# Kernel tuning notes

Hardware: AMD Instinct MI355X
Metric: run time of the kernel (lower is better)

Reference implementation:

```python
import jax, jax.numpy as jnp
import numpy as np

N_NODES = 8192
K = 64


def setup_inputs() -> dict:
    key = jax.random.key(0)
    k1, k2 = jax.random.split(key)
    A = jax.random.normal(k1, (N_NODES, N_NODES), dtype=jnp.float32)
    idx = jax.random.randint(k2, (N_NODES,), 0, N_NODES, dtype=jnp.int64)
    return {"A": A, "idx": idx}


def reference(A, idx):
    # adj = relu(A)
    adj = jax.nn.relu(A)
    # per-row top-k indices (dim=1), then scatter a 0/1 mask and multiply
    _, ind = jax.lax.top_k(adj, K)  # ind: [N, K]
    rows = jnp.arange(adj.shape[0], dtype=ind.dtype)[:, None]  # [N, 1]
    mask = jnp.zeros_like(adj).at[rows, ind].set(1.0)
    return adj * mask
```

## Files before the change

### kernel.cpp

```cpp
#include <hip/hip_runtime.h>
#include <stdint.h>


constexpr int N      = 8192;
constexpr int K      = 64;
constexpr int BLOCK  = 256;
constexpr int VPT    = N / BLOCK;
constexpr int V4     = VPT / 4;
constexpr int CAP    = 1536;
constexpr int EQ_CAP = 256;

__device__ __forceinline__ uint32_t wave_reduce_add(uint32_t x) {
    #pragma unroll
    for (int d = 32; d >= 1; d >>= 1) x += __shfl_down(x, d, 64);
    return x;
}

__device__ __forceinline__ void scan_pick(const uint32_t* hist256,
                                          uint32_t* s_prefix, uint32_t* s_k,
                                          int shift, int lane) {
    uint32_t k  = *s_k;
    uint32_t h0 = hist256[4 * lane + 0];
    uint32_t h1 = hist256[4 * lane + 1];
    uint32_t h2 = hist256[4 * lane + 2];
    uint32_t h3 = hist256[4 * lane + 3];
    uint32_t suf = h0 + h1 + h2 + h3;
    #pragma unroll
    for (int d = 1; d < 64; d <<= 1) {
        uint32_t o = __shfl_down(suf, d, 64);
        if (lane + d < 64) suf += o;
    }
    unsigned long long m = __ballot(suf >= k);
    int cl = 63 - __builtin_clzll(m);
    if (lane == cl) {
        uint32_t S0 = suf, S1 = S0 - h0, S2 = S1 - h1, S3 = S2 - h2;
        int b; uint32_t Sb, hb;
        if      (S3 >= k) { b = 3; Sb = S3; hb = h3; }
        else if (S2 >= k) { b = 2; Sb = S2; hb = h2; }
        else if (S1 >= k) { b = 1; Sb = S1; hb = h1; }
        else              { b = 0; Sb = S0; hb = h0; }
        *s_prefix |= (uint32_t)(4 * lane + b) << shift;
        *s_k = k - (Sb - hb);
    }
}

__global__ __launch_bounds__(BLOCK) void topk_row_kernel(
    const float* __restrict__ A, float* __restrict__ out)
{
    __shared__ uint32_t hist[4][256];
    __shared__ uint32_t list[CAP];
    __shared__ uint32_t s_eq[EQ_CAP];
    __shared__ uint32_t s_rb[4][5];
    __shared__ uint32_t s_rmax[4];
    __shared__ uint32_t s_prefix, s_k, s_cnt, s_listcnt, s_C, s_ecut, s_mode, s_max;

    const int tid  = threadIdx.x;
    const int wave = tid >> 6;
    const int lane = tid & 63;
    const int row  = blockIdx.x;

    const float4* rowp = reinterpret_cast<const float4*>(A + (size_t)row * N);
    float4*       outp = reinterpret_cast<float4*>(out + (size_t)row * N);

    uint32_t v[VPT];
    #pragma unroll
    for (int j = 0; j < V4; ++j) {
        float4 f = rowp[tid + j * BLOCK];
        v[4*j+0] = (f.x > 0.f) ? __float_as_uint(f.x) : 0u;
        v[4*j+1] = (f.y > 0.f) ? __float_as_uint(f.y) : 0u;
        v[4*j+2] = (f.z > 0.f) ? __float_as_uint(f.z) : 0u;
        v[4*j+3] = (f.w > 0.f) ? __float_as_uint(f.w) : 0u;
    }
    if (tid == 0) { s_listcnt = 0; s_cnt = 0; }

    uint32_t mx = 0;
    #pragma unroll
    for (int j = 0; j < VPT; ++j) mx = (v[j] > mx) ? v[j] : mx;
    #pragma unroll
    for (int d = 32; d >= 1; d >>= 1) {
        uint32_t o = __shfl_down(mx, d, 64);
        mx = (o > mx) ? o : mx;
    }
    if (lane == 0) s_rmax[wave] = mx;
    __syncthreads();
    if (tid == 0) {
        uint32_t m = s_rmax[0];
        m = (s_rmax[1] > m) ? s_rmax[1] : m;
        m = (s_rmax[2] > m) ? s_rmax[2] : m;
        m = (s_rmax[3] > m) ? s_rmax[3] : m;
        s_max = m;
    }
    __syncthreads();
    const uint32_t expM = s_max >> 23;

    uint32_t b0 = 0, b1 = 0, b2 = 0, b3 = 0, cpos = 0;
    #pragma unroll
    for (int j = 0; j < VPT; ++j) {
        uint32_t x = v[j];
        if (x != 0u) {
            uint32_t d = expM - (x >> 23);
            cpos += 1u;
            b0 += (d == 0u); b1 += (d == 1u); b2 += (d == 2u); b3 += (d == 3u);
        }
    }
    b0 = wave_reduce_add(b0); b1 = wave_reduce_add(b1);
    b2 = wave_reduce_add(b2); b3 = wave_reduce_add(b3);
    cpos = wave_reduce_add(cpos);
    if (lane == 0) {
        s_rb[wave][0] = b0; s_rb[wave][1] = b1; s_rb[wave][2] = b2;
        s_rb[wave][3] = b3; s_rb[wave][4] = cpos;
    }
    __syncthreads();
    if (tid == 0) {
        uint32_t B[5];
        #pragma unroll
        for (int c = 0; c < 5; ++c)
            B[c] = s_rb[0][c] + s_rb[1][c] + s_rb[2][c] + s_rb[3][c];
        if (B[4] < (uint32_t)K) {
            s_mode = 1;
        } else {
            s_mode = 0;
            uint32_t cum = 0; int jf = -1;
            #pragma unroll
            for (int j = 0; j < 4; ++j) {
                cum += B[j];
                if (jf < 0 && cum >= (uint32_t)K) jf = j;
            }
            if (jf >= 0) {
                uint32_t c2 = 0;
                for (int j = 0; j <= jf; ++j) c2 += B[j];
                s_C = c2; s_ecut = expM - (uint32_t)jf;
            } else {
                s_C = 0;
            }
        }
    }
    __syncthreads();

    if (s_mode == 1) {
        #pragma unroll
        for (int j = 0; j < V4; ++j) {
            float4 o;
            o.x = __uint_as_float(v[4*j+0]); o.y = __uint_as_float(v[4*j+1]);
            o.z = __uint_as_float(v[4*j+2]); o.w = __uint_as_float(v[4*j+3]);
            outp[tid + j * BLOCK] = o;
        }
        return;
    }

    if (s_C == 0) {
        uint32_t ecut = (expM > 7u) ? (expM - 7u) : 0u;
        for (;;) {
            __syncthreads();
            uint32_t lc = 0;
            #pragma unroll
            for (int j = 0; j < VPT; ++j)
                lc += (v[j] != 0u && (v[j] >> 23) >= ecut) ? 1u : 0u;
            lc = wave_reduce_add(lc);
            if (lane == 0) s_rb[wave][0] = lc;
            __syncthreads();
            if (tid == 0) {
                s_C = s_rb[0][0] + s_rb[1][0] + s_rb[2][0] + s_rb[3][0];
                s_ecut = ecut;
            }
            __syncthreads();
            if (s_C >= (uint32_t)K || ecut == 0u) break;
            ecut = (ecut > 4u) ? (ecut - 4u) : 0u;
        }
    }
    __syncthreads();
    const uint32_t C    = s_C;
    const uint32_t ecut = s_ecut;

    #pragma unroll
    for (int c = 0; c < 4; ++c) hist[c][tid] = 0;
    if (tid == 0) { s_prefix = 0; s_k = K; }
    __syncthreads();

    if (C <= (uint32_t)CAP) {
        uint32_t lc = 0;
        #pragma unroll
        for (int j = 0; j < VPT; ++j)
            lc += (v[j] != 0u && (v[j] >> 23) >= ecut) ? 1u : 0u;
        uint32_t incl = lc;
        #pragma unroll
        for (int d = 1; d < 64; d <<= 1) {
            uint32_t t = __shfl_up(incl, d, 64);
            if (lane >= d) incl += t;
        }
        uint32_t baseV = 0;
        if (lane == 63) baseV = atomicAdd(&s_listcnt, incl);
        uint32_t base = __shfl(baseV, 63, 64);
        uint32_t pos  = base + (incl - lc);
        #pragma unroll
        for (int j = 0; j < VPT; ++j) {
            uint32_t x = v[j];
            if (x != 0u && (x >> 23) >= ecut) list[pos++] = x;
        }
        __syncthreads();

        for (uint32_t i = tid; i < C; i += BLOCK)
            atomicAdd(&hist[wave][list[i] >> 24], 1u);
        __syncthreads();
        hist[0][tid] = hist[0][tid] + hist[1][tid] + hist[2][tid] + hist[3][tid];
        __syncthreads();
        if (wave == 0) scan_pick(hist[0], &s_prefix, &s_k, 24, lane);
        __syncthreads();

        for (int shift = 16; shift >= 0; shift -= 8) {
            const uint32_t prefix = s_prefix;
            #pragma unroll
            for (int c = 0; c < 4; ++c) hist[c][tid] = 0;
            __syncthreads();
            const uint32_t himask = 0xFFFFFFFFu << (shift + 8);
            for (uint32_t i = tid; i < C; i += BLOCK) {
                uint32_t x = list[i];
                if ((x & himask) == prefix)
                    atomicAdd(&hist[wave][(x >> shift) & 255u], 1u);
            }
            __syncthreads();
            hist[0][tid] = hist[0][tid] + hist[1][tid] + hist[2][tid] + hist[3][tid];
            __syncthreads();
            if (wave == 0) scan_pick(hist[0], &s_prefix, &s_k, shift, lane);
            __syncthreads();
        }
    } else {
        #pragma unroll
        for (int j = 0; j < VPT; ++j) {
            uint32_t x = v[j];
            if (x) atomicAdd(&hist[wave][x >> 24], 1u);
        }
        __syncthreads();
        hist[0][tid] = hist[0][tid] + hist[1][tid] + hist[2][tid] + hist[3][tid];
        __syncthreads();
        if (wave == 0) scan_pick(hist[0], &s_prefix, &s_k, 24, lane);
        __syncthreads();

        for (int shift = 16; shift >= 0; shift -= 8) {
            const uint32_t prefix = s_prefix;
            #pragma unroll
            for (int c = 0; c < 4; ++c) hist[c][tid] = 0;
            __syncthreads();
            const uint32_t himask = 0xFFFFFFFFu << (shift + 8);
            #pragma unroll
            for (int j = 0; j < VPT; ++j) {
                uint32_t x = v[j];
                if ((x & himask) == prefix)
                    atomicAdd(&hist[wave][(x >> shift) & 255u], 1u);
            }
            __syncthreads();
            hist[0][tid] = hist[0][tid] + hist[1][tid] + hist[2][tid] + hist[3][tid];
            __syncthreads();
            if (wave == 0) scan_pick(hist[0], &s_prefix, &s_k, shift, lane);
            __syncthreads();
        }
    }

    const uint32_t T    = s_prefix;
    const uint32_t need = s_k;
    const float    Tf   = __uint_as_float(T);

    #pragma unroll
    for (int j = 0; j < V4; ++j) {
        const int base = (tid + j * BLOCK) * 4;
        float4 o;
        float* oc = &o.x;
        #pragma unroll
        for (int c = 0; c < 4; ++c) {
            uint32_t x = v[4*j+c];
            float val = 0.f;
            if (x > T) {
                val = __uint_as_float(x);
            } else if (x == T) {
                uint32_t p = atomicAdd(&s_cnt, 1u);
                if (p < (uint32_t)EQ_CAP) s_eq[p] = (uint32_t)(base + c);
            }
            oc[c] = val;
        }
        outp[tid + j * BLOCK] = o;
    }
    __syncthreads();

    if (tid == 0) {
        uint32_t cnt = s_cnt < (uint32_t)EQ_CAP ? s_cnt : (uint32_t)EQ_CAP;
        for (uint32_t n = 0; n < need; ++n) {
            uint32_t best = 0xFFFFFFFFu, bi = 0;
            for (uint32_t i = 0; i < cnt; ++i)
                if (s_eq[i] < best) { best = s_eq[i]; bi = i; }
            if (best != 0xFFFFFFFFu) {
                s_eq[bi] = 0xFFFFFFFFu;
                out[(size_t)row * N + best] = Tf;
            }
        }
    }
}

extern "C" void kernel_launch(void* const* d_in, const int* in_sizes, int n_in,
                              void* d_out, int out_size, void* d_ws, size_t ws_size,
                              hipStream_t stream) {
    const float* A = (const float*)d_in[0];
    float* out = (float*)d_out;
    topk_row_kernel<<<N, BLOCK, 0, stream>>>(A, out);
}
```

Baseline: 442.9 us.

## Replace candidate radix passes with rank-counting threshold selection and 512-thread blocks

The small-candidate path now finds the k-th largest threshold by having each thread count how many list entries exceed its own candidate, replacing three radix-histogram passes and their barriers. Blocks grow to 512 threads with occupancy hints, row loads become nontemporal, and the per-wave reductions are folded into shared atomics with packed 16-bit counters. The cost is O(C) comparisons per thread over shared memory, and the candidate cap is lowered to 1024 so the rank path handles at most two candidates per thread.

```diff
diff --git a/kernel.cpp b/kernel.cpp
--- a/kernel.cpp
+++ b/kernel.cpp
@@ -4,11 +4,13 @@
 
 constexpr int N      = 8192;
 constexpr int K      = 64;
-constexpr int BLOCK  = 256;
+constexpr int BLOCK  = 512;
 constexpr int VPT    = N / BLOCK;
 constexpr int V4     = VPT / 4;
-constexpr int CAP    = 1536;
+constexpr int CAP    = 1024;
 constexpr int EQ_CAP = 256;
+
+typedef float  fx4 __attribute__((ext_vector_type(4)));
 
 __device__ __forceinline__ uint32_t wave_reduce_add(uint32_t x) {
     #pragma unroll
@@ -44,34 +46,39 @@
     }
 }
 
-__global__ __launch_bounds__(BLOCK) void topk_row_kernel(
+__global__ __launch_bounds__(BLOCK, 6) void topk_row_kernel(
     const float* __restrict__ A, float* __restrict__ out)
 {
+    __shared__ uint32_t list[CAP];
     __shared__ uint32_t hist[4][256];
-    __shared__ uint32_t list[CAP];
     __shared__ uint32_t s_eq[EQ_CAP];
-    __shared__ uint32_t s_rb[4][5];
-    __shared__ uint32_t s_rmax[4];
-    __shared__ uint32_t s_prefix, s_k, s_cnt, s_listcnt, s_C, s_ecut, s_mode, s_max;
+    __shared__ uint32_t s_wred[8];
+    __shared__ uint32_t s_B[5];
+    __shared__ uint32_t s_max, s_listcnt, s_cnt, s_mode, s_C, s_ecut, s_T, s_need;
 
     const int tid  = threadIdx.x;
     const int wave = tid >> 6;
     const int lane = tid & 63;
     const int row  = blockIdx.x;
 
-    const float4* rowp = reinterpret_cast<const float4*>(A + (size_t)row * N);
-    float4*       outp = reinterpret_cast<float4*>(out + (size_t)row * N);
+    const fx4* rowp = reinterpret_cast<const fx4*>(A + (size_t)row * N);
+    float4*    outp = reinterpret_cast<float4*>(out + (size_t)row * N);
+
+    if (tid == 0) {
+        s_max = 0; s_listcnt = 0; s_cnt = 0; s_mode = 0;
+        s_T = 0xFFFFFFFFu; s_need = 0;
+    }
+    if (tid < 5) s_B[tid] = 0;
 
     uint32_t v[VPT];
     #pragma unroll
     for (int j = 0; j < V4; ++j) {
-        float4 f = rowp[tid + j * BLOCK];
+        fx4 f = __builtin_nontemporal_load(&rowp[tid + j * BLOCK]);
         v[4*j+0] = (f.x > 0.f) ? __float_as_uint(f.x) : 0u;
         v[4*j+1] = (f.y > 0.f) ? __float_as_uint(f.y) : 0u;
         v[4*j+2] = (f.z > 0.f) ? __float_as_uint(f.z) : 0u;
         v[4*j+3] = (f.w > 0.f) ? __float_as_uint(f.w) : 0u;
     }
-    if (tid == 0) { s_listcnt = 0; s_cnt = 0; }
 
     uint32_t mx = 0;
     #pragma unroll
@@ -81,58 +88,48 @@
         uint32_t o = __shfl_down(mx, d, 64);
         mx = (o > mx) ? o : mx;
     }
-    if (lane == 0) s_rmax[wave] = mx;
+    __syncthreads();
+    if (lane == 0) atomicMax(&s_max, mx);
+    __syncthreads();
+    const uint32_t expM = s_max >> 23;
+
+    {
+        uint32_t p01 = 0, p23 = 0, cp = 0;
+        #pragma unroll
+        for (int j = 0; j < VPT; ++j) {
+            uint32_t x = v[j];
+            if (x != 0u) {
+                uint32_t d = expM - (x >> 23);
+                cp  += 1u;
+                p01 += (d == 0u ? 1u : 0u) + (d == 1u ? 0x10000u : 0u);
+                p23 += (d == 2u ? 1u : 0u) + (d == 3u ? 0x10000u : 0u);
+            }
+        }
+        p01 = wave_reduce_add(p01);
+        p23 = wave_reduce_add(p23);
+        cp  = wave_reduce_add(cp);
+        if (lane == 0) {
+            atomicAdd(&s_B[0], p01 & 0xFFFFu);
+            atomicAdd(&s_B[1], p01 >> 16);
+            atomicAdd(&s_B[2], p23 & 0xFFFFu);
+            atomicAdd(&s_B[3], p23 >> 16);
+            atomicAdd(&s_B[4], cp);
+        }
+    }
     __syncthreads();
     if (tid == 0) {
-        uint32_t m = s_rmax[0];
-        m = (s_rmax[1] > m) ? s_rmax[1] : m;
-        m = (s_rmax[2] > m) ? s_rmax[2] : m;
-        m = (s_rmax[3] > m) ? s_rmax[3] : m;
-        s_max = m;
-    }
-    __syncthreads();
-    const uint32_t expM = s_max >> 23;
-
-    uint32_t b0 = 0, b1 = 0, b2 = 0, b3 = 0, cpos = 0;
-    #pragma unroll
-    for (int j = 0; j < VPT; ++j) {
-        uint32_t x = v[j];
-        if (x != 0u) {
-            uint32_t d = expM - (x >> 23);
-            cpos += 1u;
-            b0 += (d == 0u); b1 += (d == 1u); b2 += (d == 2u); b3 += (d == 3u);
-        }
-    }
-    b0 = wave_reduce_add(b0); b1 = wave_reduce_add(b1);
-    b2 = wave_reduce_add(b2); b3 = wave_reduce_add(b3);
-    cpos = wave_reduce_add(cpos);
-    if (lane == 0) {
-        s_rb[wave][0] = b0; s_rb[wave][1] = b1; s_rb[wave][2] = b2;
-        s_rb[wave][3] = b3; s_rb[wave][4] = cpos;
-    }
-    __syncthreads();
-    if (tid == 0) {
-        uint32_t B[5];
-        #pragma unroll
-        for (int c = 0; c < 5; ++c)
-            B[c] = s_rb[0][c] + s_rb[1][c] + s_rb[2][c] + s_rb[3][c];
-        if (B[4] < (uint32_t)K) {
+        if (s_B[4] < (uint32_t)K) {
             s_mode = 1;
         } else {
-            s_mode = 0;
             uint32_t cum = 0; int jf = -1;
             #pragma unroll
             for (int j = 0; j < 4; ++j) {
-                cum += B[j];
-                if (jf < 0 && cum >= (uint32_t)K) jf = j;
-            }
-            if (jf >= 0) {
-                uint32_t c2 = 0;
-                for (int j = 0; j <= jf; ++j) c2 += B[j];
-                s_C = c2; s_ecut = expM - (uint32_t)jf;
-            } else {
-                s_C = 0;
-            }
+                cum += s_B[j];
+                if (jf < 0 && cum >= (uint32_t)K) {
+                    jf = j; s_C = cum; s_ecut = expM - (uint32_t)j;
+                }
+            }
+            if (jf < 0) s_mode = 2;
         }
     }
     __syncthreads();
@@ -148,34 +145,30 @@
         return;
     }
 
-    if (s_C == 0) {
-        uint32_t ecut = (expM > 7u) ? (expM - 7u) : 0u;
+    if (s_mode == 2) {
+        uint32_t ec = (expM > 7u) ? (expM - 7u) : 0u;
         for (;;) {
             __syncthreads();
             uint32_t lc = 0;
             #pragma unroll
             for (int j = 0; j < VPT; ++j)
-                lc += (v[j] != 0u && (v[j] >> 23) >= ecut) ? 1u : 0u;
+                lc += (v[j] != 0u && (v[j] >> 23) >= ec) ? 1u : 0u;
             lc = wave_reduce_add(lc);
-            if (lane == 0) s_rb[wave][0] = lc;
+            if (lane == 0) s_wred[wave] = lc;
             __syncthreads();
             if (tid == 0) {
-                s_C = s_rb[0][0] + s_rb[1][0] + s_rb[2][0] + s_rb[3][0];
-                s_ecut = ecut;
-            }
-            __syncthreads();
-            if (s_C >= (uint32_t)K || ecut == 0u) break;
-            ecut = (ecut > 4u) ? (ecut - 4u) : 0u;
-        }
-    }
-    __syncthreads();
+                uint32_t c = 0;
+                #pragma unroll
+                for (int w = 0; w < 8; ++w) c += s_wred[w];
+                s_C = c; s_ecut = ec;
+            }
+            __syncthreads();
+            if (s_C >= (uint32_t)K || ec == 0u) break;
+            ec = (ec > 8u) ? (ec - 8u) : 0u;
+        }
+    }
     const uint32_t C    = s_C;
     const uint32_t ecut = s_ecut;
-
-    #pragma unroll
-    for (int c = 0; c < 4; ++c) hist[c][tid] = 0;
-    if (tid == 0) { s_prefix = 0; s_k = K; }
-    __syncthreads();
 
     if (C <= (uint32_t)CAP) {
         uint32_t lc = 0;
@@ -197,67 +190,65 @@
             uint32_t x = v[j];
             if (x != 0u && (x >> 23) >= ecut) list[pos++] = x;
         }
-        __syncthreads();
-
-        for (uint32_t i = tid; i < C; i += BLOCK)
-            atomicAdd(&hist[wave][list[i] >> 24], 1u);
-        __syncthreads();
-        hist[0][tid] = hist[0][tid] + hist[1][tid] + hist[2][tid] + hist[3][tid];
-        __syncthreads();
-        if (wave == 0) scan_pick(hist[0], &s_prefix, &s_k, 24, lane);
-        __syncthreads();
-
-        for (int shift = 16; shift >= 0; shift -= 8) {
-            const uint32_t prefix = s_prefix;
-            #pragma unroll
-            for (int c = 0; c < 4; ++c) hist[c][tid] = 0;
-            __syncthreads();
-            const uint32_t himask = 0xFFFFFFFFu << (shift + 8);
-            for (uint32_t i = tid; i < C; i += BLOCK) {
-                uint32_t x = list[i];
-                if ((x & himask) == prefix)
-                    atomicAdd(&hist[wave][(x >> shift) & 255u], 1u);
-            }
-            __syncthreads();
-            hist[0][tid] = hist[0][tid] + hist[1][tid] + hist[2][tid] + hist[3][tid];
-            __syncthreads();
-            if (wave == 0) scan_pick(hist[0], &s_prefix, &s_k, shift, lane);
-            __syncthreads();
-        }
+        const uint32_t Cp = (C + 3u) & ~3u;
+        for (uint32_t i = C + tid; i < Cp; i += BLOCK) list[i] = 0u;
+        __syncthreads();
+
+        uint32_t x0 = (tid < (int)C)          ? list[tid]          : 0u;
+        uint32_t x1 = (tid + BLOCK < (int)C)  ? list[tid + BLOCK]  : 0u;
+        uint32_t c0 = 0, c1 = 0;
+        const uint4* l4 = reinterpret_cast<const uint4*>(list);
+        const uint32_t n4 = Cp >> 2;
+        for (uint32_t i = 0; i < n4; ++i) {
+            uint4 y = l4[i];
+            c0 += (y.x > x0) + (y.y > x0) + (y.z > x0) + (y.w > x0);
+            c1 += (y.x > x1) + (y.y > x1) + (y.z > x1) + (y.w > x1);
+        }
+        if (x0 != 0u && c0 < (uint32_t)K) atomicMin(&s_T, x0);
+        if (x1 != 0u && c1 < (uint32_t)K) atomicMin(&s_T, x1);
+        __syncthreads();
+        const uint32_t Tv = s_T;
+        if (x0 == Tv && x0 != 0u) s_need = (uint32_t)K - c0;
+        if (x1 == Tv && x1 != 0u) s_need = (uint32_t)K - c1;
+        __syncthreads();
     } else {
+        if (tid == 0) { s_T = 0; s_need = K; }
+        if (tid < 256) { hist[0][tid]=0; hist[1][tid]=0; hist[2][tid]=0; hist[3][tid]=0; }
+        __syncthreads();
         #pragma unroll
         for (int j = 0; j < VPT; ++j) {
             uint32_t x = v[j];
-            if (x) atomicAdd(&hist[wave][x >> 24], 1u);
-        }
-        __syncthreads();
-        hist[0][tid] = hist[0][tid] + hist[1][tid] + hist[2][tid] + hist[3][tid];
-        __syncthreads();
-        if (wave == 0) scan_pick(hist[0], &s_prefix, &s_k, 24, lane);
+            if (x) atomicAdd(&hist[wave & 3][x >> 24], 1u);
+        }
+        __syncthreads();
+        if (tid < 256)
+            hist[0][tid] = hist[0][tid] + hist[1][tid] + hist[2][tid] + hist[3][tid];
+        __syncthreads();
+        if (wave == 0) scan_pick(hist[0], &s_T, &s_need, 24, lane);
         __syncthreads();
 
         for (int shift = 16; shift >= 0; shift -= 8) {
-            const uint32_t prefix = s_prefix;
-            #pragma unroll
-            for (int c = 0; c < 4; ++c) hist[c][tid] = 0;
+            const uint32_t prefix = s_T;
+            if (tid < 256) { hist[0][tid]=0; hist[1][tid]=0; hist[2][tid]=0; hist[3][tid]=0; }
             __syncthreads();
             const uint32_t himask = 0xFFFFFFFFu << (shift + 8);
             #pragma unroll
             for (int j = 0; j < VPT; ++j) {
                 uint32_t x = v[j];
                 if ((x & himask) == prefix)
-                    atomicAdd(&hist[wave][(x >> shift) & 255u], 1u);
-            }
-            __syncthreads();
-            hist[0][tid] = hist[0][tid] + hist[1][tid] + hist[2][tid] + hist[3][tid];
-            __syncthreads();
-            if (wave == 0) scan_pick(hist[0], &s_prefix, &s_k, shift, lane);
-            __syncthreads();
-        }
-    }
-
-    const uint32_t T    = s_prefix;
-    const uint32_t need = s_k;
+                    atomicAdd(&hist[wave & 3][(x >> shift) & 255u], 1u);
+            }
+            __syncthreads();
+            if (tid < 256)
+                hist[0][tid] = hist[0][tid] + hist[1][tid] + hist[2][tid] + hist[3][tid];
+            __syncthreads();
+            if (wave == 0) scan_pick(hist[0], &s_T, &s_need, shift, lane);
+            __syncthreads();
+        }
+    }
+
+    const uint32_t T    = s_T;
+    const uint32_t need = s_need;
     const float    Tf   = __uint_as_float(T);
 
     #pragma unroll
```

Result: slower. 485.7 us (+9.7%).
